# Performance work log

Hardware: AMD Instinct MI355X
Metric: run time of the kernel (lower is better)

The kernel has to match this reference:

```python
import jax, jax.numpy as jnp
import numpy as np

N_NODES = 50000
N_EDGES = 800000
F_IN = 128
HID = 128
N_CLASSES = 2
N_GRAPHS = 500
NEG_SLOPE = 0.2


def setup_inputs() -> dict:
    key = jax.random.key(0)
    ks = jax.random.split(key, 16)
    inp = {
        "x": jax.random.normal(ks[0], (N_NODES, F_IN), dtype=jnp.float32),
        "edge_index": jax.random.randint(ks[1], (2, N_EDGES), 0, N_NODES, dtype=jnp.int64),
        "batch": jnp.sort(jax.random.randint(ks[2], (N_NODES,), 0, N_GRAPHS, dtype=jnp.int64)),
    }
    dims = [(F_IN, HID), (HID, HID), (HID, HID)]
    for i, (din, dout) in enumerate(dims, start=1):
        s = 1.0 / np.sqrt(din)
        inp[f"W{i}"] = jax.random.uniform(ks[3 * i], (din, dout), minval=-s, maxval=s, dtype=jnp.float32)
        inp[f"a_src{i}"] = jax.random.uniform(ks[3 * i + 1], (dout,), minval=-s, maxval=s, dtype=jnp.float32)
        inp[f"a_dst{i}"] = jax.random.uniform(ks[3 * i + 2], (dout,), minval=-s, maxval=s, dtype=jnp.float32)
        inp[f"b{i}"] = jnp.zeros((dout,), dtype=jnp.float32)
    s = 1.0 / np.sqrt(HID)
    inp["W_lin"] = jax.random.uniform(ks[12], (HID, N_CLASSES), minval=-s, maxval=s, dtype=jnp.float32)
    inp["b_lin"] = jax.random.uniform(ks[13], (N_CLASSES,), minval=-s, maxval=s, dtype=jnp.float32)
    return inp


def gat_conv(x, src, dst, W, a_src, a_dst, b, n_nodes):
    # single-head PyG GATConv (heads=1, concat), self-loops already in src/dst
    h = x @ W                                   # [N, dout]
    alpha_src = h @ a_src                       # [N]
    alpha_dst = h @ a_dst                       # [N]
    e = jax.nn.leaky_relu(alpha_src[src] + alpha_dst[dst], NEG_SLOPE)  # [E]
    # segment softmax over edges grouped by destination node
    m = jax.ops.segment_max(e, dst, num_segments=n_nodes)
    ex = jnp.exp(e - m[dst])
    denom = jax.ops.segment_sum(ex, dst, num_segments=n_nodes)
    alpha = ex / denom[dst]                     # [E]
    out = jax.ops.segment_sum(h[src] * alpha[:, None], dst, num_segments=n_nodes)
    return out + b


def reference(x, edge_index, batch, W1, a_src1, a_dst1, b1, W2, a_src2, a_dst2, b2,
              W3, a_src3, a_dst3, b3, W_lin, b_lin):
    n = x.shape[0]
    loops = jnp.arange(n, dtype=edge_index.dtype)
    src = jnp.concatenate([edge_index[0], loops])
    dst = jnp.concatenate([edge_index[1], loops])

    h = jax.nn.relu(gat_conv(x, src, dst, W1, a_src1, a_dst1, b1, n))
    h = jax.nn.relu(gat_conv(h, src, dst, W2, a_src2, a_dst2, b2, n))
    h = gat_conv(h, src, dst, W3, a_src3, a_dst3, b3, n)

    # global mean pool over graphs
    sums = jax.ops.segment_sum(h, batch, num_segments=N_GRAPHS)       # [G, HID]
    counts = jax.ops.segment_sum(jnp.ones((n,), h.dtype), batch, num_segments=N_GRAPHS)
    pooled = sums / jnp.maximum(counts, 1.0)[:, None]
    # dropout is identity in eval mode
    return pooled @ W_lin + b_lin
```

## Files before the change

kernel.cpp:

```cpp
#include <hip/hip_runtime.h>
#include <math.h>

#define N_NODES  50000
#define N_EDGES  800000
#define FDIM     128
#define N_GRAPHS 500
#define NEG_SLOPE 0.2f
#define EN_TOTAL (N_EDGES + N_NODES)
#define SCAN_NB ((N_NODES + 255) / 256)
#define GEMM_TILES (N_NODES / 16)
#define WT_COLS 144
#define PREP_PLANE_BLOCKS 1024
#define PREP_GRID (3 + PREP_PLANE_BLOCKS + SCAN_NB)

typedef short bf16x8 __attribute__((ext_vector_type(8)));
typedef float f32x4 __attribute__((ext_vector_type(4)));

static __device__ __forceinline__ float lrelu(float x) {
    return x >= 0.f ? x : NEG_SLOPE * x;
}
static __device__ __forceinline__ unsigned short f2bf(float v) {
    unsigned int u = __float_as_uint(v);
    u += 0x7fffu + ((u >> 16) & 1u);
    return (unsigned short)(u >> 16);
}
static __device__ __forceinline__ float bf2f(unsigned short s) {
    return __uint_as_float(((unsigned int)s) << 16);
}

__global__ __launch_bounds__(256) void prep_all(
    const float* __restrict__ X,
    const float* __restrict__ W0, const float* __restrict__ W1,
    const float* __restrict__ W2,
    const float* __restrict__ as0, const float* __restrict__ as1,
    const float* __restrict__ as2,
    const float* __restrict__ ad0, const float* __restrict__ ad1,
    const float* __restrict__ ad2,
    unsigned short* __restrict__ WT,
    unsigned short* __restrict__ PHI, unsigned short* __restrict__ PLO,
    int* __restrict__ cnt)
{
    __shared__ float wa[256];
    const int b = blockIdx.x, tid = threadIdx.x;

    if (b < 3) {
        const float* W  = (b == 0) ? W0  : (b == 1) ? W1  : W2;
        const float* As = (b == 0) ? as0 : (b == 1) ? as1 : as2;
        const float* Ad = (b == 0) ? ad0 : (b == 1) ? ad1 : ad2;
        unsigned short* hi = WT + (size_t)b * 2 * WT_COLS * FDIM;
        unsigned short* lo = hi + WT_COLS * FDIM;
        {
            const int k = tid & 127;
            const float* av = (tid < 128) ? As : Ad;
            float s = 0.f;
            for (int c = 0; c < 128; ++c) s += W[k * FDIM + c] * av[c];
            wa[tid] = s;
        }
        __syncthreads();
        for (int i = tid; i < FDIM * FDIM; i += 256) {
            const int k = i >> 7, c = i & 127;
            const float v = W[i];
            const unsigned short h = f2bf(v);
            hi[c * FDIM + k] = h;
            lo[c * FDIM + k] = f2bf(v - bf2f(h));
        }
        for (int k = tid; k < FDIM; k += 256) {
            const float vs = wa[k], vd = wa[128 + k];
            const unsigned short hs = f2bf(vs), hd = f2bf(vd);
            hi[128 * FDIM + k] = hs; lo[128 * FDIM + k] = f2bf(vs - bf2f(hs));
            hi[129 * FDIM + k] = hd; lo[129 * FDIM + k] = f2bf(vd - bf2f(hd));
        }
        for (int i = tid; i < 14 * FDIM; i += 256) {
            hi[130 * FDIM + i] = 0;
            lo[130 * FDIM + i] = 0;
        }
    } else if (b < 3 + PREP_PLANE_BLOCKS) {
        const int total = N_NODES * FDIM / 4;
        for (int i = (b - 3) * 256 + tid; i < total; i += PREP_PLANE_BLOCKS * 256) {
            const float4 v = ((const float4*)X)[i];
            ushort4 h4, l4;
            h4.x = f2bf(v.x); l4.x = f2bf(v.x - bf2f(h4.x));
            h4.y = f2bf(v.y); l4.y = f2bf(v.y - bf2f(h4.y));
            h4.z = f2bf(v.z); l4.z = f2bf(v.z - bf2f(h4.z));
            h4.w = f2bf(v.w); l4.w = f2bf(v.w - bf2f(h4.w));
            ((ushort4*)PHI)[i] = h4;
            ((ushort4*)PLO)[i] = l4;
        }
    } else {
        const int i = (b - 3 - PREP_PLANE_BLOCKS) * 256 + tid;
        if (i < N_NODES) cnt[i] = 0;
    }
}

__global__ __launch_bounds__(256) void gemm_mfma6(
    const unsigned short* __restrict__ PHI, const unsigned short* __restrict__ PLO,
    const unsigned short* __restrict__ WThi, const unsigned short* __restrict__ WTlo,
    unsigned short* __restrict__ Hb, float* __restrict__ asrcN, float* __restrict__ adstN)
{
    __shared__ unsigned short sH[2][16 * 128];
    __shared__ unsigned short sL[2][16 * 128];

    const int tid = threadIdx.x, wv = tid >> 6, lane = tid & 63;
    const int r16 = lane & 15, g = lane >> 4;
    const int t0 = wv * 2;

    bf16x8 bh[2][4], bl[2][4];
    #pragma unroll
    for (int tt = 0; tt < 2; ++tt) {
        const int c = (t0 + tt) * 16 + r16;
        #pragma unroll
        for (int cc = 0; cc < 4; ++cc) {
            bh[tt][cc] = *(const bf16x8*)(WThi + c * FDIM + cc * 32 + 8 * g);
            bl[tt][cc] = *(const bf16x8*)(WTlo + c * FDIM + cc * 32 + 8 * g);
        }
    }
    const unsigned short* WThiE = WThi + (128 + r16) * FDIM + 8 * g;
    const unsigned short* WTloE = WTlo + (128 + r16) * FDIM + 8 * g;

    const int srow = wv * 4 + (lane >> 4);
    const int sslot = lane & 15;
    const int ldsOfs = srow * 128 + ((sslot ^ (srow & 7)) * 8);
    const size_t gOfs0 = (size_t)srow * FDIM + sslot * 8;

    int tile = blockIdx.x;
    {
        const size_t go = (size_t)tile * 16 * FDIM + gOfs0;
        *(uint4*)(&sH[0][ldsOfs]) = *(const uint4*)(PHI + go);
        *(uint4*)(&sL[0][ldsOfs]) = *(const uint4*)(PLO + go);
    }
    __syncthreads();

    int cur = 0, rot = 0;
    for (; tile < GEMM_TILES; tile += gridDim.x, ++rot) {
        const int nxt = tile + (int)gridDim.x;
        if (nxt < GEMM_TILES) {
            const size_t go = (size_t)nxt * 16 * FDIM + gOfs0;
            *(uint4*)(&sH[cur ^ 1][ldsOfs]) = *(const uint4*)(PHI + go);
            *(uint4*)(&sL[cur ^ 1][ldsOfs]) = *(const uint4*)(PLO + go);
        }

        bf16x8 ah[4], al[4];
        #pragma unroll
        for (int cc = 0; cc < 4; ++cc) {
            const int p = (cc * 4 + g) ^ (r16 & 7);
            const int ofs = r16 * 128 + p * 8;
            ah[cc] = *(const bf16x8*)(&sH[cur][ofs]);
            al[cc] = *(const bf16x8*)(&sL[cur][ofs]);
        }

        f32x4 acc0 = {0.f, 0.f, 0.f, 0.f}, acc1 = {0.f, 0.f, 0.f, 0.f};
        #pragma unroll
        for (int cc = 0; cc < 4; ++cc) {
            acc0 = __builtin_amdgcn_mfma_f32_16x16x32_bf16(ah[cc], bh[0][cc], acc0, 0, 0, 0);
            acc1 = __builtin_amdgcn_mfma_f32_16x16x32_bf16(ah[cc], bh[1][cc], acc1, 0, 0, 0);
            acc0 = __builtin_amdgcn_mfma_f32_16x16x32_bf16(al[cc], bh[0][cc], acc0, 0, 0, 0);
            acc1 = __builtin_amdgcn_mfma_f32_16x16x32_bf16(al[cc], bh[1][cc], acc1, 0, 0, 0);
            acc0 = __builtin_amdgcn_mfma_f32_16x16x32_bf16(ah[cc], bl[0][cc], acc0, 0, 0, 0);
            acc1 = __builtin_amdgcn_mfma_f32_16x16x32_bf16(ah[cc], bl[1][cc], acc1, 0, 0, 0);
        }

        const int m0 = tile * 16;
        const int rowb = m0 + 4 * g;
        #pragma unroll
        for (int r = 0; r < 4; ++r) {
            Hb[(size_t)(rowb + r) * FDIM + (t0 + 0) * 16 + r16] = f2bf(acc0[r]);
            Hb[(size_t)(rowb + r) * FDIM + (t0 + 1) * 16 + r16] = f2bf(acc1[r]);
        }

        if (wv == ((tile + rot) & 3)) {
            f32x4 acce = {0.f, 0.f, 0.f, 0.f};
            #pragma unroll
            for (int cc = 0; cc < 4; ++cc) {
                const bf16x8 bhe = *(const bf16x8*)(WThiE + cc * 32);
                const bf16x8 ble = *(const bf16x8*)(WTloE + cc * 32);
                acce = __builtin_amdgcn_mfma_f32_16x16x32_bf16(ah[cc], bhe, acce, 0, 0, 0);
                acce = __builtin_amdgcn_mfma_f32_16x16x32_bf16(al[cc], bhe, acce, 0, 0, 0);
                acce = __builtin_amdgcn_mfma_f32_16x16x32_bf16(ah[cc], ble, acce, 0, 0, 0);
            }
            if (r16 == 0) {
                #pragma unroll
                for (int r = 0; r < 4; ++r) asrcN[rowb + r] = acce[r];
            } else if (r16 == 1) {
                #pragma unroll
                for (int r = 0; r < 4; ++r) adstN[rowb + r] = acce[r];
            }
        }

        __syncthreads();
        cur ^= 1;
    }
}

__global__ void count_edges(const int* __restrict__ ei, int* __restrict__ cnt) {
    int i = blockIdx.x * 256 + threadIdx.x;
    if (i < EN_TOTAL) {
        int d = (i < N_EDGES) ? ei[N_EDGES + i] : (i - N_EDGES);
        atomicAdd(&cnt[d], 1);
    }
}

__global__ __launch_bounds__(256) void scan_block(const int* __restrict__ cnt,
                                                  int* __restrict__ off,
                                                  int* __restrict__ blockSums) {
    __shared__ int s[256];
    const int i = blockIdx.x * 256 + threadIdx.x;
    s[threadIdx.x] = (i < N_NODES) ? cnt[i] : 0;
    __syncthreads();
    #pragma unroll
    for (int d = 1; d < 256; d <<= 1) {
        int t = (threadIdx.x >= d) ? s[threadIdx.x - d] : 0;
        __syncthreads();
        s[threadIdx.x] += t;
        __syncthreads();
    }
    if (i < N_NODES) off[i + 1] = s[threadIdx.x];
    if (threadIdx.x == 255) blockSums[blockIdx.x] = s[255];
}

__global__ __launch_bounds__(256) void scan_sums(int* __restrict__ blockSums) {
    __shared__ int s[256];
    s[threadIdx.x] = (threadIdx.x < SCAN_NB) ? blockSums[threadIdx.x] : 0;
    __syncthreads();
    #pragma unroll
    for (int d = 1; d < 256; d <<= 1) {
        int t = (threadIdx.x >= d) ? s[threadIdx.x - d] : 0;
        __syncthreads();
        s[threadIdx.x] += t;
        __syncthreads();
    }
    if (threadIdx.x < SCAN_NB)
        blockSums[threadIdx.x] = (threadIdx.x == 0) ? 0 : s[threadIdx.x - 1];
}

__global__ __launch_bounds__(256) void add_base(int* __restrict__ off,
                                                const int* __restrict__ blockSums,
                                                int* __restrict__ offm) {
    const int i = blockIdx.x * 256 + threadIdx.x;
    if (i < N_NODES) {
        const int v = off[i + 1] + blockSums[blockIdx.x];
        off[i + 1] = v;
        offm[i + 1] = v;
    }
    if (i == 0) { off[0] = 0; offm[0] = 0; }
}

__global__ void scatter_edges(const int* __restrict__ ei, int* __restrict__ offm,
                              int* __restrict__ srcs) {
    int i = blockIdx.x * 256 + threadIdx.x;
    if (i < EN_TOTAL) {
        int s, d;
        if (i < N_EDGES) { s = ei[i]; d = ei[N_EDGES + i]; }
        else             { s = d = i - N_EDGES; }
        int p = atomicAdd(&offm[d], 1);
        srcs[p] = s;
    }
}

__global__ __launch_bounds__(256) void gat_aggregate(
    const unsigned short* __restrict__ Hb, const int* __restrict__ off,
    const int* __restrict__ srcs,
    const float* __restrict__ asrcN, const float* __restrict__ adstN,
    const float* __restrict__ bias,
    unsigned short* __restrict__ PHI, unsigned short* __restrict__ PLO,
    float* __restrict__ OUTF, int mode)
{
    const int wave = threadIdx.x >> 6, lane = threadIdx.x & 63;
    const int grp = lane >> 3, fl = lane & 7;

    for (int n = blockIdx.x * 4 + wave; n < N_NODES; n += gridDim.x * 4) {
        const int s0 = off[n], s1 = off[n + 1];
        const int deg = s1 - s0;
        const float ad = adstN[n];

        float e_reg = -1e30f;
        float m = -1e30f;
        for (int j = s0 + lane; j < s1; j += 64) {
            float e = lrelu(asrcN[srcs[j]] + ad);
            if (j - s0 < 64) e_reg = e;
            m = fmaxf(m, e);
        }
        #pragma unroll
        for (int o = 32; o; o >>= 1) m = fmaxf(m, __shfl_xor(m, o));

        float4 a0 = {0,0,0,0}, a1 = {0,0,0,0}, a2 = {0,0,0,0}, a3 = {0,0,0,0};
        float dn = 0.f;
        const unsigned short* Hf = Hb + (size_t)fl * 16;
        for (int j = s0 + grp; j < s1; j += 8) {
            const int s = srcs[j];
            const float ex = (deg <= 64)
                ? __expf(__shfl(e_reg, j - s0) - m)
                : __expf(lrelu(asrcN[s] + ad) - m);
            dn += ex;
            const uint4* hp = (const uint4*)(Hf + (size_t)s * FDIM);
            const uint4 u0 = hp[0], u1 = hp[1];
            a0.x += ex * __uint_as_float(u0.x << 16);
            a0.y += ex * __uint_as_float(u0.x & 0xffff0000u);
            a0.z += ex * __uint_as_float(u0.y << 16);
            a0.w += ex * __uint_as_float(u0.y & 0xffff0000u);
            a1.x += ex * __uint_as_float(u0.z << 16);
            a1.y += ex * __uint_as_float(u0.z & 0xffff0000u);
            a1.z += ex * __uint_as_float(u0.w << 16);
            a1.w += ex * __uint_as_float(u0.w & 0xffff0000u);
            a2.x += ex * __uint_as_float(u1.x << 16);
            a2.y += ex * __uint_as_float(u1.x & 0xffff0000u);
            a2.z += ex * __uint_as_float(u1.y << 16);
            a2.w += ex * __uint_as_float(u1.y & 0xffff0000u);
            a3.x += ex * __uint_as_float(u1.z << 16);
            a3.y += ex * __uint_as_float(u1.z & 0xffff0000u);
            a3.z += ex * __uint_as_float(u1.w << 16);
            a3.w += ex * __uint_as_float(u1.w & 0xffff0000u);
        }

        #pragma unroll
        for (int o = 8; o <= 32; o <<= 1) {
            dn  += __shfl_xor(dn, o);
            a0.x += __shfl_xor(a0.x, o); a0.y += __shfl_xor(a0.y, o);
            a0.z += __shfl_xor(a0.z, o); a0.w += __shfl_xor(a0.w, o);
            a1.x += __shfl_xor(a1.x, o); a1.y += __shfl_xor(a1.y, o);
            a1.z += __shfl_xor(a1.z, o); a1.w += __shfl_xor(a1.w, o);
            a2.x += __shfl_xor(a2.x, o); a2.y += __shfl_xor(a2.y, o);
            a2.z += __shfl_xor(a2.z, o); a2.w += __shfl_xor(a2.w, o);
            a3.x += __shfl_xor(a3.x, o); a3.y += __shfl_xor(a3.y, o);
            a3.z += __shfl_xor(a3.z, o); a3.w += __shfl_xor(a3.w, o);
        }

        if (grp == 0) {
            const float rd = 1.f / dn;
            const float4* bp = (const float4*)(bias + fl * 16);
            float4 ov[4] = {a0, a1, a2, a3};
            #pragma unroll
            for (int q = 0; q < 4; ++q) {
                const float4 b4 = bp[q];
                float4 o4;
                o4.x = ov[q].x * rd + b4.x; o4.y = ov[q].y * rd + b4.y;
                o4.z = ov[q].z * rd + b4.z; o4.w = ov[q].w * rd + b4.w;
                if (mode == 0) {
                    o4.x = fmaxf(o4.x, 0.f); o4.y = fmaxf(o4.y, 0.f);
                    o4.z = fmaxf(o4.z, 0.f); o4.w = fmaxf(o4.w, 0.f);
                    ushort4 h4, l4;
                    h4.x = f2bf(o4.x); l4.x = f2bf(o4.x - bf2f(h4.x));
                    h4.y = f2bf(o4.y); l4.y = f2bf(o4.y - bf2f(h4.y));
                    h4.z = f2bf(o4.z); l4.z = f2bf(o4.z - bf2f(h4.z));
                    h4.w = f2bf(o4.w); l4.w = f2bf(o4.w - bf2f(h4.w));
                    const size_t base = (size_t)n * FDIM + fl * 16 + q * 4;
                    *(ushort4*)(PHI + base) = h4;
                    *(ushort4*)(PLO + base) = l4;
                } else {
                    *(float4*)(OUTF + (size_t)n * FDIM + fl * 16 + q * 4) = o4;
                }
            }
        }
    }
}

__global__ __launch_bounds__(256) void pool_linear2(
    const float* __restrict__ H, const int* __restrict__ batch,
    const float* __restrict__ Wlin, const float* __restrict__ blin,
    float* __restrict__ out)
{
    const int g = blockIdx.x, tid = threadIdx.x;
    const int rl = tid >> 5, fq = tid & 31;

    int a = 0, b = N_NODES;
    while (a < b) { int mid = (a + b) >> 1; if (batch[mid] < g) a = mid + 1; else b = mid; }
    const int lo = a;
    b = N_NODES;
    while (a < b) { int mid = (a + b) >> 1; if (batch[mid] <= g) a = mid + 1; else b = mid; }
    const int hi = a;

    float4 acc = {0.f, 0.f, 0.f, 0.f};
    for (int n = lo + rl; n < hi; n += 8) {
        const float4 v = *(const float4*)(H + (size_t)n * FDIM + fq * 4);
        acc.x += v.x; acc.y += v.y; acc.z += v.z; acc.w += v.w;
    }
    __shared__ float4 s[8][32];
    s[rl][fq] = acc;
    __syncthreads();

    if (tid < 32) {
        float4 t = s[0][fq];
        #pragma unroll
        for (int r = 1; r < 8; ++r) {
            const float4 v = s[r][fq];
            t.x += v.x; t.y += v.y; t.z += v.z; t.w += v.w;
        }
        const float inv = 1.f / fmaxf((float)(hi - lo), 1.f);
        t.x *= inv; t.y *= inv; t.z *= inv; t.w *= inv;
        float d0 = t.x * Wlin[(fq * 4 + 0) * 2 + 0] + t.y * Wlin[(fq * 4 + 1) * 2 + 0]
                 + t.z * Wlin[(fq * 4 + 2) * 2 + 0] + t.w * Wlin[(fq * 4 + 3) * 2 + 0];
        float d1 = t.x * Wlin[(fq * 4 + 0) * 2 + 1] + t.y * Wlin[(fq * 4 + 1) * 2 + 1]
                 + t.z * Wlin[(fq * 4 + 2) * 2 + 1] + t.w * Wlin[(fq * 4 + 3) * 2 + 1];
        #pragma unroll
        for (int o = 1; o <= 16; o <<= 1) {
            d0 += __shfl_xor(d0, o);
            d1 += __shfl_xor(d1, o);
        }
        if (fq == 0) {
            out[g * 2 + 0] = d0 + blin[0];
            out[g * 2 + 1] = d1 + blin[1];
        }
    }
}

extern "C" void kernel_launch(void* const* d_in, const int* in_sizes, int n_in,
                              void* d_out, int out_size, void* d_ws, size_t ws_size,
                              hipStream_t stream)
{
    const float* x     = (const float*)d_in[0];
    const int*   ei    = (const int*)d_in[1];
    const int*   batch = (const int*)d_in[2];
    const float* W[3]    = {(const float*)d_in[3],  (const float*)d_in[7],  (const float*)d_in[11]};
    const float* avs[3]  = {(const float*)d_in[4],  (const float*)d_in[8],  (const float*)d_in[12]};
    const float* avd[3]  = {(const float*)d_in[5],  (const float*)d_in[9],  (const float*)d_in[13]};
    const float* bias[3] = {(const float*)d_in[6],  (const float*)d_in[10], (const float*)d_in[14]};
    const float* Wlin = (const float*)d_in[15];
    const float* blin = (const float*)d_in[16];
    float* out = (float*)d_out;

    char* w = (char*)d_ws;
    unsigned short* PHI = (unsigned short*)w; w += (size_t)N_NODES * FDIM * 2;
    unsigned short* PLO = (unsigned short*)w; w += (size_t)N_NODES * FDIM * 2;
    float* hOf = (float*)PHI;
    unsigned short* Hb = (unsigned short*)w; w += (size_t)N_NODES * FDIM * 2;
    float* attn  = (float*)w; w += 2 * 200192;
    int*   off   = (int*)w;   w += 200192;
    int*   offm  = (int*)w;   w += 200192;
    int*   cnt   = (int*)w;   w += 200192;
    int*   bsum  = (int*)w;   w += 4096;
    int*   srcs  = (int*)w;   w += (size_t)EN_TOTAL * 4;
    unsigned short* WT = (unsigned short*)w; w += (size_t)3 * 2 * WT_COLS * FDIM * 2;
    float* asrcN = attn;
    float* adstN = attn + N_NODES;

    prep_all<<<PREP_GRID, 256, 0, stream>>>(x, W[0], W[1], W[2],
                                            avs[0], avs[1], avs[2],
                                            avd[0], avd[1], avd[2],
                                            WT, PHI, PLO, cnt);

    count_edges<<<(EN_TOTAL + 255) / 256, 256, 0, stream>>>(ei, cnt);
    scan_block<<<SCAN_NB, 256, 0, stream>>>(cnt, off, bsum);
    scan_sums<<<1, 256, 0, stream>>>(bsum);
    add_base<<<SCAN_NB, 256, 0, stream>>>(off, bsum, offm);
    scatter_edges<<<(EN_TOTAL + 255) / 256, 256, 0, stream>>>(ei, offm, srcs);

    for (int l = 0; l < 3; ++l) {
        const unsigned short* WThi = WT + (size_t)l * 2 * WT_COLS * FDIM;
        const unsigned short* WTlo = WThi + WT_COLS * FDIM;
        gemm_mfma6<<<1024, 256, 0, stream>>>(PHI, PLO, WThi, WTlo, Hb, asrcN, adstN);
        gat_aggregate<<<2048, 256, 0, stream>>>(Hb, off, srcs, asrcN, adstN, bias[l],
                                                PHI, PLO, hOf, (l < 2) ? 0 : 1);
    }

    pool_linear2<<<N_GRAPHS, 256, 0, stream>>>(hOf, batch, Wlin, blin, out);
}
```

Measured before the change: 350.3 us.

## Replace global-atomic edge scatter with two-pass bucketed binning

The CSR build no longer scatters each edge with a global atomic on its destination's offset. Edges are first binned into 16 coarse destination buckets using per-block shared histograms, with one global atomic per bucket per block. A second kernel then places edges within each bucket using shared-memory cursors. This cuts global atomic contention and random writes, at the cost of an extra pass over an intermediate buffer. The place step runs on only 16 blocks, which limits parallelism.

```diff
diff --git a/kernel.cpp b/kernel.cpp
--- a/kernel.cpp
+++ b/kernel.cpp
@@ -12,6 +12,9 @@
 #define WT_COLS 144
 #define PREP_PLANE_BLOCKS 1024
 #define PREP_GRID (3 + PREP_PLANE_BLOCKS + SCAN_NB)
+#define NBUCK 16
+#define BSHIFT 12
+#define BWIDTH 4096
 
 typedef short bf16x8 __attribute__((ext_vector_type(8)));
 typedef float f32x4 __attribute__((ext_vector_type(4)));
@@ -234,25 +237,63 @@
 
 __global__ __launch_bounds__(256) void add_base(int* __restrict__ off,
                                                 const int* __restrict__ blockSums,
-                                                int* __restrict__ offm) {
+                                                int* __restrict__ bcur) {
     const int i = blockIdx.x * 256 + threadIdx.x;
     if (i < N_NODES) {
         const int v = off[i + 1] + blockSums[blockIdx.x];
         off[i + 1] = v;
-        offm[i + 1] = v;
-    }
-    if (i == 0) { off[0] = 0; offm[0] = 0; }
-}
-
-__global__ void scatter_edges(const int* __restrict__ ei, int* __restrict__ offm,
-                              int* __restrict__ srcs) {
-    int i = blockIdx.x * 256 + threadIdx.x;
-    if (i < EN_TOTAL) {
-        int s, d;
-        if (i < N_EDGES) { s = ei[i]; d = ei[N_EDGES + i]; }
-        else             { s = d = i - N_EDGES; }
-        int p = atomicAdd(&offm[d], 1);
-        srcs[p] = s;
+        if (((i + 1) & (BWIDTH - 1)) == 0) bcur[(i + 1) >> BSHIFT] = v;
+    }
+    if (i == 0) { off[0] = 0; bcur[0] = 0; }
+}
+
+__global__ __launch_bounds__(256) void bin_edges(
+    const int* __restrict__ ei, int* __restrict__ bcur,
+    unsigned int* __restrict__ ebuf)
+{
+    __shared__ int hist[NBUCK], base[NBUCK], rank[NBUCK];
+    const int tid = threadIdx.x;
+    for (int t0 = blockIdx.x * 256; t0 < EN_TOTAL; t0 += gridDim.x * 256) {
+        const int i = t0 + tid;
+        int b = -1; unsigned int payload = 0;
+        if (i < EN_TOTAL) {
+            int s, d;
+            if (i < N_EDGES) { s = ei[i]; d = ei[N_EDGES + i]; }
+            else             { s = d = i - N_EDGES; }
+            b = d >> BSHIFT;
+            payload = ((unsigned int)(d & (BWIDTH - 1)) << 17) | (unsigned int)s;
+        }
+        if (tid < NBUCK) { hist[tid] = 0; rank[tid] = 0; }
+        __syncthreads();
+        if (b >= 0) atomicAdd(&hist[b], 1);
+        __syncthreads();
+        if (tid < NBUCK) base[tid] = hist[tid] ? atomicAdd(&bcur[tid], hist[tid]) : 0;
+        __syncthreads();
+        if (b >= 0) {
+            const int r = atomicAdd(&rank[b], 1);
+            ebuf[base[b] + r] = payload;
+        }
+        __syncthreads();
+    }
+}
+
+__global__ __launch_bounds__(512) void place_edges(
+    const int* __restrict__ off, const unsigned int* __restrict__ ebuf,
+    int* __restrict__ srcs)
+{
+    __shared__ int lcur[BWIDTH];
+    const int b = blockIdx.x;
+    const int d0 = b << BSHIFT;
+    if (d0 >= N_NODES) return;
+    const int d1 = min(d0 + BWIDTH, N_NODES);
+    const int nd = d1 - d0;
+    for (int i = threadIdx.x; i < nd; i += 512) lcur[i] = off[d0 + i];
+    __syncthreads();
+    const int start = off[d0], end = off[d1];
+    for (int i = start + threadIdx.x; i < end; i += 512) {
+        const unsigned int e = ebuf[i];
+        const int p = atomicAdd(&lcur[e >> 17], 1);
+        srcs[p] = (int)(e & 0x1FFFFu);
     }
 }
 
@@ -424,10 +465,11 @@
     unsigned short* Hb = (unsigned short*)w; w += (size_t)N_NODES * FDIM * 2;
     float* attn  = (float*)w; w += 2 * 200192;
     int*   off   = (int*)w;   w += 200192;
-    int*   offm  = (int*)w;   w += 200192;
     int*   cnt   = (int*)w;   w += 200192;
     int*   bsum  = (int*)w;   w += 4096;
+    int*   bcur  = (int*)w;   w += 256;
     int*   srcs  = (int*)w;   w += (size_t)EN_TOTAL * 4;
+    unsigned int* ebuf = (unsigned int*)w; w += (size_t)EN_TOTAL * 4;
     unsigned short* WT = (unsigned short*)w; w += (size_t)3 * 2 * WT_COLS * FDIM * 2;
     float* asrcN = attn;
     float* adstN = attn + N_NODES;
@@ -440,8 +482,9 @@
     count_edges<<<(EN_TOTAL + 255) / 256, 256, 0, stream>>>(ei, cnt);
     scan_block<<<SCAN_NB, 256, 0, stream>>>(cnt, off, bsum);
     scan_sums<<<1, 256, 0, stream>>>(bsum);
-    add_base<<<SCAN_NB, 256, 0, stream>>>(off, bsum, offm);
-    scatter_edges<<<(EN_TOTAL + 255) / 256, 256, 0, stream>>>(ei, offm, srcs);
+    add_base<<<SCAN_NB, 256, 0, stream>>>(off, bsum, bcur);
+    bin_edges<<<1024, 256, 0, stream>>>(ei, bcur, ebuf);
+    place_edges<<<NBUCK, 512, 0, stream>>>(off, ebuf, srcs);
 
     for (int l = 0; l < 3; ++l) {
         const unsigned short* WThi = WT + (size_t)l * 2 * WT_COLS * FDIM;
```

After: 407.8 us. 16.4% more time.

## Replace global-atomic CSR build with two-level bucketed counting sort

Applied to the files above, without the earlier changes.

Builds the destination-sorted edge list with a two-pass bucket sort instead of per-edge global atomics. Edges are first binned into 196 coarse buckets of 256 destination nodes using shared-memory histograms, then each bucket is sorted locally in shared memory to produce offsets and source ids. This cuts the five CSR kernels to four and replaces heavily contended global atomics with shared-memory atomics. It costs an extra pass over the edge list and an extra intermediate buffer, and it also changes the order of edges within each destination's segment.

```diff
diff --git a/kernel.cpp b/kernel.cpp
--- a/kernel.cpp
+++ b/kernel.cpp
@@ -7,11 +7,15 @@
 #define N_GRAPHS 500
 #define NEG_SLOPE 0.2f
 #define EN_TOTAL (N_EDGES + N_NODES)
-#define SCAN_NB ((N_NODES + 255) / 256)
 #define GEMM_TILES (N_NODES / 16)
 #define WT_COLS 144
 #define PREP_PLANE_BLOCKS 1024
-#define PREP_GRID (3 + PREP_PLANE_BLOCKS + SCAN_NB)
+#define PREP_GRID (3 + PREP_PLANE_BLOCKS + 1)
+#define BSHIFT 8
+#define BWIDTH 256
+#define NBUCK ((N_NODES + BWIDTH - 1) / BWIDTH)
+#define BIN_BATCH 8192
+#define BIN_BLOCKS ((EN_TOTAL + BIN_BATCH - 1) / BIN_BATCH)
 
 typedef short bf16x8 __attribute__((ext_vector_type(8)));
 typedef float f32x4 __attribute__((ext_vector_type(4)));
@@ -38,7 +42,7 @@
     const float* __restrict__ ad2,
     unsigned short* __restrict__ WT,
     unsigned short* __restrict__ PHI, unsigned short* __restrict__ PLO,
-    int* __restrict__ cnt)
+    int* __restrict__ bcnt)
 {
     __shared__ float wa[256];
     const int b = blockIdx.x, tid = threadIdx.x;
@@ -87,8 +91,7 @@
             ((ushort4*)PLO)[i] = l4;
         }
     } else {
-        const int i = (b - 3 - PREP_PLANE_BLOCKS) * 256 + tid;
-        if (i < N_NODES) cnt[i] = 0;
+        if (tid < 256) bcnt[tid] = 0;
     }
 }
 
@@ -191,68 +194,108 @@
     }
 }
 
-__global__ void count_edges(const int* __restrict__ ei, int* __restrict__ cnt) {
-    int i = blockIdx.x * 256 + threadIdx.x;
-    if (i < EN_TOTAL) {
-        int d = (i < N_EDGES) ? ei[N_EDGES + i] : (i - N_EDGES);
-        atomicAdd(&cnt[d], 1);
-    }
-}
-
-__global__ __launch_bounds__(256) void scan_block(const int* __restrict__ cnt,
-                                                  int* __restrict__ off,
-                                                  int* __restrict__ blockSums) {
+__global__ __launch_bounds__(256) void bucket_count(const int* __restrict__ ei,
+                                                    int* __restrict__ bcnt) {
+    __shared__ int hist[NBUCK];
+    const int tid = threadIdx.x;
+    if (tid < NBUCK) hist[tid] = 0;
+    __syncthreads();
+    const int i0 = blockIdx.x * BIN_BATCH;
+    const int i1 = min(i0 + BIN_BATCH, EN_TOTAL);
+    for (int i = i0 + tid; i < i1; i += 256) {
+        const int d = (i < N_EDGES) ? ei[N_EDGES + i] : (i - N_EDGES);
+        atomicAdd(&hist[d >> BSHIFT], 1);
+    }
+    __syncthreads();
+    if (tid < NBUCK && hist[tid]) atomicAdd(&bcnt[tid], hist[tid]);
+}
+
+__global__ __launch_bounds__(256) void bucket_scan(const int* __restrict__ bcnt,
+                                                   int* __restrict__ bbase,
+                                                   int* __restrict__ bcur,
+                                                   int* __restrict__ off) {
     __shared__ int s[256];
-    const int i = blockIdx.x * 256 + threadIdx.x;
-    s[threadIdx.x] = (i < N_NODES) ? cnt[i] : 0;
+    const int tid = threadIdx.x;
+    s[tid] = (tid < NBUCK) ? bcnt[tid] : 0;
     __syncthreads();
     #pragma unroll
     for (int d = 1; d < 256; d <<= 1) {
-        int t = (threadIdx.x >= d) ? s[threadIdx.x - d] : 0;
-        __syncthreads();
-        s[threadIdx.x] += t;
-        __syncthreads();
-    }
-    if (i < N_NODES) off[i + 1] = s[threadIdx.x];
-    if (threadIdx.x == 255) blockSums[blockIdx.x] = s[255];
-}
-
-__global__ __launch_bounds__(256) void scan_sums(int* __restrict__ blockSums) {
-    __shared__ int s[256];
-    s[threadIdx.x] = (threadIdx.x < SCAN_NB) ? blockSums[threadIdx.x] : 0;
-    __syncthreads();
-    #pragma unroll
-    for (int d = 1; d < 256; d <<= 1) {
-        int t = (threadIdx.x >= d) ? s[threadIdx.x - d] : 0;
-        __syncthreads();
-        s[threadIdx.x] += t;
-        __syncthreads();
-    }
-    if (threadIdx.x < SCAN_NB)
-        blockSums[threadIdx.x] = (threadIdx.x == 0) ? 0 : s[threadIdx.x - 1];
-}
-
-__global__ __launch_bounds__(256) void add_base(int* __restrict__ off,
-                                                const int* __restrict__ blockSums,
-                                                int* __restrict__ offm) {
-    const int i = blockIdx.x * 256 + threadIdx.x;
-    if (i < N_NODES) {
-        const int v = off[i + 1] + blockSums[blockIdx.x];
-        off[i + 1] = v;
-        offm[i + 1] = v;
-    }
-    if (i == 0) { off[0] = 0; offm[0] = 0; }
-}
-
-__global__ void scatter_edges(const int* __restrict__ ei, int* __restrict__ offm,
-                              int* __restrict__ srcs) {
-    int i = blockIdx.x * 256 + threadIdx.x;
-    if (i < EN_TOTAL) {
+        int t = (tid >= d) ? s[tid - d] : 0;
+        __syncthreads();
+        s[tid] += t;
+        __syncthreads();
+    }
+    if (tid < NBUCK) {
+        const int base = (tid == 0) ? 0 : s[tid - 1];
+        bbase[tid] = base;
+        bcur[tid] = base;
+    }
+    if (tid == 0) { bbase[NBUCK] = EN_TOTAL; off[N_NODES] = EN_TOTAL; }
+}
+
+__global__ __launch_bounds__(256) void bin_edges(const int* __restrict__ ei,
+                                                 int* __restrict__ bcur,
+                                                 unsigned int* __restrict__ ebuf) {
+    __shared__ int hist[NBUCK], base[NBUCK];
+    const int tid = threadIdx.x;
+    if (tid < NBUCK) hist[tid] = 0;
+    __syncthreads();
+    const int i0 = blockIdx.x * BIN_BATCH;
+    const int i1 = min(i0 + BIN_BATCH, EN_TOTAL);
+    for (int i = i0 + tid; i < i1; i += 256) {
+        const int d = (i < N_EDGES) ? ei[N_EDGES + i] : (i - N_EDGES);
+        atomicAdd(&hist[d >> BSHIFT], 1);
+    }
+    __syncthreads();
+    if (tid < NBUCK) {
+        base[tid] = hist[tid] ? atomicAdd(&bcur[tid], hist[tid]) : 0;
+        hist[tid] = 0;
+    }
+    __syncthreads();
+    for (int i = i0 + tid; i < i1; i += 256) {
         int s, d;
         if (i < N_EDGES) { s = ei[i]; d = ei[N_EDGES + i]; }
         else             { s = d = i - N_EDGES; }
-        int p = atomicAdd(&offm[d], 1);
-        srcs[p] = s;
+        const int b = d >> BSHIFT;
+        const int r = atomicAdd(&hist[b], 1);
+        ebuf[base[b] + r] = ((unsigned int)(d & (BWIDTH - 1)) << 17) | (unsigned int)s;
+    }
+}
+
+__global__ __launch_bounds__(512) void place_edges(
+    const int* __restrict__ bbase, const unsigned int* __restrict__ ebuf,
+    int* __restrict__ off, int* __restrict__ srcs)
+{
+    __shared__ int hist[BWIDTH], scn[BWIDTH];
+    const int b = blockIdx.x, tid = threadIdx.x;
+    const int d0 = b << BSHIFT;
+    const int nd = min(BWIDTH, N_NODES - d0);
+    const int bstart = bbase[b], bend = bbase[b + 1];
+
+    if (tid < BWIDTH) hist[tid] = 0;
+    __syncthreads();
+    for (int i = bstart + tid; i < bend; i += 512)
+        atomicAdd(&hist[ebuf[i] >> 17], 1);
+    __syncthreads();
+    if (tid < BWIDTH) scn[tid] = hist[tid];
+    __syncthreads();
+    #pragma unroll
+    for (int d = 1; d < BWIDTH; d <<= 1) {
+        int t = (tid < BWIDTH && tid >= d) ? scn[tid - d] : 0;
+        __syncthreads();
+        if (tid < BWIDTH) scn[tid] += t;
+        __syncthreads();
+    }
+    if (tid < nd) {
+        const int start = bstart + (tid ? scn[tid - 1] : 0);
+        off[d0 + tid] = start;
+        hist[tid] = start;
+    }
+    __syncthreads();
+    for (int i = bstart + tid; i < bend; i += 512) {
+        const unsigned int e = ebuf[i];
+        const int p = atomicAdd(&hist[e >> 17], 1);
+        srcs[p] = (int)(e & 0x1FFFFu);
     }
 }
 
@@ -424,10 +467,11 @@
     unsigned short* Hb = (unsigned short*)w; w += (size_t)N_NODES * FDIM * 2;
     float* attn  = (float*)w; w += 2 * 200192;
     int*   off   = (int*)w;   w += 200192;
-    int*   offm  = (int*)w;   w += 200192;
-    int*   cnt   = (int*)w;   w += 200192;
-    int*   bsum  = (int*)w;   w += 4096;
+    int*   bcnt  = (int*)w;   w += 1024;
+    int*   bbase = (int*)w;   w += 1024;
+    int*   bcur  = (int*)w;   w += 1024;
     int*   srcs  = (int*)w;   w += (size_t)EN_TOTAL * 4;
+    unsigned int* ebuf = (unsigned int*)w; w += (size_t)EN_TOTAL * 4;
     unsigned short* WT = (unsigned short*)w; w += (size_t)3 * 2 * WT_COLS * FDIM * 2;
     float* asrcN = attn;
     float* adstN = attn + N_NODES;
@@ -435,13 +479,12 @@
     prep_all<<<PREP_GRID, 256, 0, stream>>>(x, W[0], W[1], W[2],
                                             avs[0], avs[1], avs[2],
                                             avd[0], avd[1], avd[2],
-                                            WT, PHI, PLO, cnt);
-
-    count_edges<<<(EN_TOTAL + 255) / 256, 256, 0, stream>>>(ei, cnt);
-    scan_block<<<SCAN_NB, 256, 0, stream>>>(cnt, off, bsum);
-    scan_sums<<<1, 256, 0, stream>>>(bsum);
-    add_base<<<SCAN_NB, 256, 0, stream>>>(off, bsum, offm);
-    scatter_edges<<<(EN_TOTAL + 255) / 256, 256, 0, stream>>>(ei, offm, srcs);
+                                            WT, PHI, PLO, bcnt);
+
+    bucket_count<<<BIN_BLOCKS, 256, 0, stream>>>(ei, bcnt);
+    bucket_scan<<<1, 256, 0, stream>>>(bcnt, bbase, bcur, off);
+    bin_edges<<<BIN_BLOCKS, 256, 0, stream>>>(ei, bcur, ebuf);
+    place_edges<<<NBUCK, 512, 0, stream>>>(bbase, ebuf, off, srcs);
 
     for (int l = 0; l < 3; ++l) {
         const unsigned short* WThi = WT + (size_t)l * 2 * WT_COLS * FDIM;
```

New measurement: 298.7 us. 1.17x faster.
